# Optimization experiments

Measured on AMD Instinct MI355X. Metric: run time of the kernel, lower is better.

## Reference

```python
import jax, jax.numpy as jnp
import numpy as np

F, E, B = 30, 16, 4096
IN = F * E          # 480 = sum of embed dims
H1, H2 = 1024, 512  # fcn_dims
K = 32              # low-rank adapter k
HH = 512            # hyper hidden dim
D = 3               # domain_num
V = 10000           # vocab per field
EPS = 1e-5


def _bn(h, g, b):
    # BatchNorm1d in training mode: biased batch stats
    mu = h.mean(0)
    var = h.var(0)
    return g * (h - mu) * jax.lax.rsqrt(var + EPS) + b


def setup_inputs() -> dict:
    key = jax.random.key(0)
    ks = jax.random.split(key, 10)
    x = jax.random.randint(ks[0], (F, B), 0, V)
    # last row of x is the domain id, must be in [0, D)
    x = x.at[-1].set(jax.random.randint(ks[1], (B,), 0, D))
    w = lambda k_, s: jax.random.normal(k_, s, jnp.float32) * 0.02
    return {
        "x": x,
        "emb_tables": w(ks[2], (F, V, E)),
        # per-domain MLP (stacked over D): Linear/BN x2 + final Linear(H2->1)
        "dW0": w(ks[3], (D, IN, H1)), "db0": jnp.zeros((D, H1)),
        "dg0": jnp.ones((D, H1)), "dbt0": jnp.zeros((D, H1)),
        "dW1": w(ks[4], (D, H1, H2)), "db1": jnp.zeros((D, H2)),
        "dg1": jnp.ones((D, H2)), "dbt1": jnp.zeros((D, H2)),
        "dWo": w(ks[5], (D, H2, 1)), "dbo": jnp.zeros((D, 1)),
        # hyper_net: Linear+BN+ReLU (IN->HH), Linear+BN+ReLU (HH->K*K)
        "hW0": w(ks[6], (IN, HH)), "hb0": jnp.zeros((HH,)),
        "hg0": jnp.ones((HH,)), "hbt0": jnp.zeros((HH,)),
        "hW1": w(ks[7], (HH, K * K)), "hb1": jnp.zeros((K * K,)),
        "hg1": jnp.ones((K * K,)), "hbt1": jnp.zeros((K * K,)),
        # low-rank factors (torch inits these to ones)
        "u0": jnp.ones((H2, K)), "u1": jnp.ones((32, K)),
        "v0": jnp.ones((K, 32)), "v1": jnp.ones((K, H2)),
        "bl0": jnp.zeros((32,)), "bl1": jnp.zeros((H2,)),
        "gamma1": jnp.ones((H2,)), "bias1": jnp.zeros((H2,)),
    }


def reference(x, emb_tables, dW0, db0, dg0, dbt0, dW1, db1, dg1, dbt1,
              dWo, dbo, hW0, hb0, hg0, hbt0, hW1, hb1, hg1, hbt1,
              u0, u1, v0, v1, bl0, bl1, gamma1, bias1):
    domain_id = x[-1]                                        # [B]
    emb = jax.vmap(lambda t, idx: t[idx])(emb_tables, x)     # [F, B, E]
    emb = emb.transpose(1, 0, 2).reshape(x.shape[1], -1)     # [B, F*E]

    # hyper-net output is identical across the domain loop -> compute once
    h = jax.nn.relu(_bn(emb @ hW0 + hb0, hg0, hbt0))
    h = jax.nn.relu(_bn(h @ hW1 + hb1, hg1, hbt1))
    hyper = h.reshape(-1, K, K)                              # [B, K, K]
    w1 = jnp.einsum('mi,bij,jn->bmn', u0, hyper, v0)         # [B, H2, 32]
    w2 = jnp.einsum('mi,bij,jn->bmn', u1, hyper, v1)         # [B, 32, H2]

    outs = []
    for d in range(D):
        di = jax.nn.relu(_bn(emb @ dW0[d] + db0[d], dg0[d], dbt0[d]))  # [B, H1]
        di = jax.nn.relu(_bn(di @ dW1[d] + db1[d], dg1[d], dbt1[d]))   # [B, H2]
        t = jax.nn.sigmoid(jnp.einsum('bf,bfj->bj', di, w1) + bl0)     # [B, 32]
        t = jnp.einsum('bf,bfj->bj', t, w2) + bl1                      # [B, H2]
        # manual batch-norm with torch.var (unbiased, ddof=1)
        mean, var = t.mean(0), t.var(0, ddof=1)
        out = gamma1 * (t - mean) / jnp.sqrt(var + EPS) + bias1
        di = out + di                                                  # residual
        outs.append(jax.nn.sigmoid(di @ dWo[d] + dbo[d]))              # [B, 1]

    final = jnp.zeros_like(outs[0])
    for d in range(D):
        final = jnp.where((domain_id == d)[:, None], outs[d], final)
    return final
```

## Files before the change

### kernel.cpp

```cpp
#include <hip/hip_runtime.h>
#include <hip/hip_bf16.h>
#include <math.h>

#define F_   30
#define E_   16
#define B_   4096
#define IN_  480
#define H1_  1024
#define H2_  512
#define K_   32
#define HH_  512
#define D_   3
#define V_   10000
#define EPS_ 1e-5f

typedef __attribute__((ext_vector_type(8))) short bf16x8;
typedef __attribute__((ext_vector_type(4))) float f32x4;
typedef __attribute__((ext_vector_type(8))) unsigned short u16x8;

__device__ __forceinline__ unsigned short f2bf(float f) {
    unsigned u = __builtin_bit_cast(unsigned, f);
    u += 0x7FFFu + ((u >> 16) & 1u);
    return (unsigned short)(u >> 16);
}
__device__ __forceinline__ float bf2f(unsigned short h) {
    return __builtin_bit_cast(float, ((unsigned)h) << 16);
}
__device__ __forceinline__ void gload_lds16(const unsigned short* g, unsigned short* l) {
    typedef unsigned int __attribute__((address_space(1))) guint;
    typedef unsigned int __attribute__((address_space(3))) luint;
    __builtin_amdgcn_global_load_lds((const guint*)g, (luint*)l, 16, 0, 0);
}

struct TransArgs {
    const float* src[9];
    unsigned short* dst[9];
    int K[9], N[9], base[9];
};
#define PREP_ZB   73
#define PREP_GA   (PREP_ZB + 960)
#define PREP_TR   (PREP_GA + 3744)
#define PREP_CV   (PREP_TR + 64)
__global__ __launch_bounds__(256) void prep_kernel(TransArgs ta,
                                                   float* __restrict__ zero_p, int zero_n,
                                                   const int* __restrict__ x,
                                                   const float* __restrict__ tables,
                                                   unsigned short* __restrict__ emb,
                                                   const float* __restrict__ v1,
                                                   unsigned short* __restrict__ v1bf) {
    __shared__ float tile[32][33];
    int blk = blockIdx.x;
    int t = threadIdx.x;
    if (blk < PREP_ZB) {
        int i = blk * 256 + t;
        if (i < zero_n) zero_p[i] = 0.f;
    } else if (blk < PREP_GA) {
        int idx = (blk - PREP_ZB) * 256 + t;
        int b = idx / (F_ * 2);
        int r = idx - b * (F_ * 2);
        int f = r >> 1, h = r & 1;
        int row = x[f * B_ + b];
        const float4* src = reinterpret_cast<const float4*>(tables + ((size_t)f * V_ + row) * E_ + h * 8);
        float4 v0 = src[0], v1v = src[1];
        u16x8 o;
        o[0]=f2bf(v0.x); o[1]=f2bf(v0.y); o[2]=f2bf(v0.z); o[3]=f2bf(v0.w);
        o[4]=f2bf(v1v.x); o[5]=f2bf(v1v.y); o[6]=f2bf(v1v.z); o[7]=f2bf(v1v.w);
        *reinterpret_cast<u16x8*>(emb + (size_t)b * IN_ + f * E_ + h * 8) = o;
    } else if (blk < PREP_TR) {
        int gblk = blk - PREP_GA;
        int seg = 0;
#pragma unroll
        for (int i = 1; i < 9; i++) if (gblk >= ta.base[i]) seg = i;
        int tix = gblk - ta.base[seg];
        int Kd = ta.K[seg], Nd = ta.N[seg];
        int tn = Nd >> 5;
        int k0 = (tix / tn) << 5;
        int n0 = (tix - (tix / tn) * tn) << 5;
        const float* src = ta.src[seg];
        unsigned short* dst = ta.dst[seg];
        int c = t & 31, rr = t >> 5;
#pragma unroll
        for (int i = 0; i < 4; i++) {
            int r = rr + i * 8;
            tile[r][c] = src[(size_t)(k0 + r) * Nd + n0 + c];
        }
        __syncthreads();
#pragma unroll
        for (int i = 0; i < 4; i++) {
            int r = rr + i * 8;
            dst[(size_t)(n0 + r) * Kd + k0 + c] = f2bf(tile[c][r]);
        }
    } else {
        int i = (blk - PREP_TR) * 256 + t;
        if (i < K_ * H2_) v1bf[i] = f2bf(v1[i]);
    }
}

struct GemmGroups {
    const unsigned short* A[4];
    const unsigned short* Bt[4];
    void* C[4];
    float* stats[4];
    int N[4], K[4], base[4], obf[4];
};
__global__ __launch_bounds__(256) void gemm_grouped(GemmGroups p) {
    __shared__ unsigned short sA[128 * 32];
    __shared__ unsigned short sB[128 * 32];
    int blk = blockIdx.x;
    int g = 0;
#pragma unroll
    for (int i = 1; i < 4; i++) if (blk >= p.base[i]) g = i;
    int tix = blk - p.base[g];
    int N = p.N[g], K = p.K[g];
    const unsigned short* A = p.A[g];
    const unsigned short* Bt = p.Bt[g];
    float* stats = p.stats[g];
    int bm = (tix & 31) << 7;
    int bn = (tix >> 5) << 7;

    int tid = threadIdx.x;
    int l = tid & 63, w = tid >> 6;
    int wr = w >> 1, wc = w & 1;
    const unsigned short* Ab = A + (size_t)bm * K;
    const unsigned short* Bb = Bt + (size_t)bn * K;
    f32x4 acc[4][4] = {};
    int n0c = tid, n1c = tid + 256;
    int r0 = n0c >> 2, lc0 = (n0c & 3) ^ ((r0 >> 1) & 3);
    int r1 = n1c >> 2, lc1 = (n1c & 3) ^ ((r1 >> 1) & 3);
    int kg = l >> 4, lr = l & 15;
    for (int k0 = 0; k0 < K; k0 += 32) {
        gload_lds16(Ab + (size_t)r0 * K + k0 + lc0 * 8, &sA[n0c * 8]);
        gload_lds16(Ab + (size_t)r1 * K + k0 + lc1 * 8, &sA[n1c * 8]);
        gload_lds16(Bb + (size_t)r0 * K + k0 + lc0 * 8, &sB[n0c * 8]);
        gload_lds16(Bb + (size_t)r1 * K + k0 + lc1 * 8, &sB[n1c * 8]);
        __syncthreads();
        bf16x8 af[4], bfr[4];
#pragma unroll
        for (int m = 0; m < 4; m++) {
            int R = (wr << 6) + (m << 4) + lr;
            af[m] = *reinterpret_cast<const bf16x8*>(&sA[R * 32 + ((kg ^ ((R >> 1) & 3)) << 3)]);
        }
#pragma unroll
        for (int n = 0; n < 4; n++) {
            int R = (wc << 6) + (n << 4) + lr;
            bfr[n] = *reinterpret_cast<const bf16x8*>(&sB[R * 32 + ((kg ^ ((R >> 1) & 3)) << 3)]);
        }
#pragma unroll
        for (int m = 0; m < 4; m++)
#pragma unroll
            for (int n = 0; n < 4; n++)
                acc[m][n] = __builtin_amdgcn_mfma_f32_16x16x32_bf16(af[m], bfr[n], acc[m][n], 0, 0, 0);
        __syncthreads();
    }
    int orow = bm + (wr << 6) + (kg << 2);
    int ocol = bn + (wc << 6) + lr;
    if (p.obf[g]) {
        unsigned short* Cb = (unsigned short*)p.C[g];
#pragma unroll
        for (int m = 0; m < 4; m++)
#pragma unroll
            for (int n = 0; n < 4; n++)
#pragma unroll
                for (int j = 0; j < 4; j++)
                    Cb[(size_t)(orow + (m << 4) + j) * N + ocol + (n << 4)] = f2bf(acc[m][n][j]);
    } else {
        float* C = (float*)p.C[g];
#pragma unroll
        for (int m = 0; m < 4; m++)
#pragma unroll
            for (int n = 0; n < 4; n++)
#pragma unroll
                for (int j = 0; j < 4; j++)
                    C[(size_t)(orow + (m << 4) + j) * N + ocol + (n << 4)] = acc[m][n][j];
    }
#pragma unroll
    for (int n = 0; n < 4; n++) {
        float s = 0.f, ss = 0.f;
#pragma unroll
        for (int m = 0; m < 4; m++)
#pragma unroll
            for (int j = 0; j < 4; j++) {
                float v = acc[m][n][j];
                s += v; ss += v * v;
            }
        s  += __shfl_xor(s, 16);  s  += __shfl_xor(s, 32);
        ss += __shfl_xor(ss, 16); ss += __shfl_xor(ss, 32);
        if (l < 16) {
            int col = bn + (wc << 6) + (n << 4) + lr;
            atomicAdd(&stats[col], s);
            atomicAdd(&stats[N + col], ss);
        }
    }
}

__global__ __launch_bounds__(256) void gemm_bf16_N32(const unsigned short* __restrict__ D1BF,
                                                     const unsigned short* __restrict__ Bt,
                                                     float* __restrict__ Afac) {
    __shared__ unsigned short sA[128 * 32];
    __shared__ unsigned short sB[32 * 32];
    int d = blockIdx.y;
    const unsigned short* A = D1BF + (size_t)d * B_ * H2_;
    float* C = Afac + (size_t)d * B_ * 32;
    const int K = 512;
    int tid = threadIdx.x;
    int l = tid & 63, w = tid >> 6;
    int bm = blockIdx.x << 7;
    const unsigned short* Ab = A + (size_t)bm * K;
    f32x4 acc[2][2] = {};
    int n0c = tid, n1c = tid + 256;
    int r0 = n0c >> 2, lc0 = (n0c & 3) ^ ((r0 >> 1) & 3);
    int r1 = n1c >> 2, lc1 = (n1c & 3) ^ ((r1 >> 1) & 3);
    int kg = l >> 4, lr = l & 15;
    for (int k0 = 0; k0 < K; k0 += 32) {
        gload_lds16(Ab + (size_t)r0 * K + k0 + lc0 * 8, &sA[n0c * 8]);
        gload_lds16(Ab + (size_t)r1 * K + k0 + lc1 * 8, &sA[n1c * 8]);
        if (tid < 128)
            gload_lds16(Bt + (size_t)r0 * K + k0 + lc0 * 8, &sB[n0c * 8]);
        __syncthreads();
        bf16x8 af[2], bfr[2];
#pragma unroll
        for (int m = 0; m < 2; m++) {
            int R = (w << 5) + (m << 4) + lr;
            af[m] = *reinterpret_cast<const bf16x8*>(&sA[R * 32 + ((kg ^ ((R >> 1) & 3)) << 3)]);
        }
#pragma unroll
        for (int n = 0; n < 2; n++) {
            int R = (n << 4) + lr;
            bfr[n] = *reinterpret_cast<const bf16x8*>(&sB[R * 32 + ((kg ^ ((R >> 1) & 3)) << 3)]);
        }
#pragma unroll
        for (int m = 0; m < 2; m++)
#pragma unroll
            for (int n = 0; n < 2; n++)
                acc[m][n] = __builtin_amdgcn_mfma_f32_16x16x32_bf16(af[m], bfr[n], acc[m][n], 0, 0, 0);
        __syncthreads();
    }
    int orow = bm + (w << 5) + (kg << 2);
#pragma unroll
    for (int m = 0; m < 2; m++)
#pragma unroll
        for (int n = 0; n < 2; n++)
#pragma unroll
            for (int j = 0; j < 4; j++)
                C[(size_t)(orow + (m << 4) + j) * 32 + (n << 4) + lr] = acc[m][n][j];
}

__global__ __launch_bounds__(256) void bn480_kernel(const unsigned short* __restrict__ Z480bf,
                                                    const float* __restrict__ stats,
                                                    const float* __restrict__ hg0,
                                                    const float* __restrict__ hbt0,
                                                    const float* __restrict__ dg0,
                                                    const float* __restrict__ dbt0,
                                                    unsigned short* __restrict__ Z0BF,
                                                    unsigned short* __restrict__ ZD0BF) {
    int idx = blockIdx.x * 256 + threadIdx.x;
    int b = idx / 448;
    int c0 = (idx - b * 448) * 8;
    const float* g;
    const float* bt;
    unsigned short* dst;
    if (c0 < 512) {
        g = hg0 + c0; bt = hbt0 + c0;
        dst = Z0BF + (size_t)b * 512 + c0;
    } else {
        int d = (c0 - 512) >> 10, cc = (c0 - 512) & 1023;
        g = dg0 + d * 1024 + cc; bt = dbt0 + d * 1024 + cc;
        dst = ZD0BF + ((size_t)d << 22) + (size_t)b * 1024 + cc;
    }
    u16x8 v = *reinterpret_cast<const u16x8*>(Z480bf + (size_t)b * 3584 + c0);
    u16x8 o;
#pragma unroll
    for (int q = 0; q < 8; q++) {
        float S = stats[c0 + q], SS = stats[3584 + c0 + q];
        float m = S * (1.f / B_);
        float var = (SS - S * m) * (1.f / B_);
        float rs = rsqrtf(var + EPS_);
        o[q] = f2bf(fmaxf(0.f, g[q] * (bf2f(v[q]) - m) * rs + bt[q]));
    }
    *reinterpret_cast<u16x8*>(dst) = o;
}

__global__ __launch_bounds__(256) void bn_l1_kernel(const float* __restrict__ Z1scr,
                                                    const float* __restrict__ SCR1,
                                                    const float* __restrict__ statsH,
                                                    const float* __restrict__ statsD1,
                                                    const float* __restrict__ hg1,
                                                    const float* __restrict__ hbt1,
                                                    const float* __restrict__ dg1,
                                                    const float* __restrict__ dbt1,
                                                    unsigned short* __restrict__ Hbf,
                                                    unsigned short* __restrict__ D1BF) {
    int gidx = blockIdx.x * 256 + threadIdx.x;
    const float* Z; const float* stats; const float* g; const float* bt;
    unsigned short* outp; int c0; int idx;
    if (gidx < 524288) {
        idx = gidx;
        c0 = (idx & 127) * 8;
        Z = Z1scr; stats = statsH; g = hg1; bt = hbt1; outp = Hbf;
    } else {
        idx = gidx - 524288;
        int row = idx >> 6;
        int d = row >> 12;
        c0 = (idx & 63) * 8;
        Z = SCR1; stats = statsD1 + d * 1024; g = dg1 + d * 512; bt = dbt1 + d * 512; outp = D1BF;
    }
    int sh = (gidx < 524288) ? 1024 : 512;
    float4 v0 = reinterpret_cast<const float4*>(Z)[(size_t)idx * 2];
    float4 v1 = reinterpret_cast<const float4*>(Z)[(size_t)idx * 2 + 1];
    float r[8] = {v0.x, v0.y, v0.z, v0.w, v1.x, v1.y, v1.z, v1.w};
    u16x8 o;
#pragma unroll
    for (int q = 0; q < 8; q++) {
        float S = stats[c0 + q], SS = stats[sh + c0 + q];
        float m = S * (1.f / B_);
        float var = (SS - S * m) * (1.f / B_);
        float rs = rsqrtf(var + EPS_);
        o[q] = f2bf(fmaxf(0.f, g[c0 + q] * (r[q] - m) * rs + bt[c0 + q]));
    }
    *reinterpret_cast<u16x8*>(outp + (size_t)idx * 8) = o;
}

__global__ __launch_bounds__(256) void adapter_core(const float* __restrict__ Afac,
                                                    const unsigned short* __restrict__ Hbf,
                                                    const float* __restrict__ v0,
                                                    const float* __restrict__ u1,
                                                    const float* __restrict__ bl0,
                                                    float* __restrict__ C2) {
    __shared__ float sv0[K_ * K_];
    __shared__ float su1[K_ * K_];
    int t = threadIdx.x;
    reinterpret_cast<float4*>(sv0)[t] = reinterpret_cast<const float4*>(v0)[t];
    reinterpret_cast<float4*>(su1)[t] = reinterpret_cast<const float4*>(u1)[t];
    __syncthreads();
    int w = t >> 6, l = t & 63;
    int i = l & 31;
    int b = blockIdx.x * 4 + w;
    float hreg[32];
#pragma unroll
    for (int k = 0; k < 32; k++) hreg[k] = bf2f(Hbf[(size_t)b * 1024 + k * 32 + i]);
    float bl0i = bl0[i];
#pragma unroll
    for (int d = 0; d < 3; d++) {
        float a = Afac[(size_t)d * 131072 + b * 32 + i];
        float c = 0.f;
#pragma unroll
        for (int k = 0; k < 32; k++) c += __shfl(a, k) * hreg[k];
        float targ = bl0i;
#pragma unroll
        for (int k = 0; k < 32; k++) targ += __shfl(c, k) * sv0[k * 32 + i];
        float tv = 1.f / (1.f + expf(-targ));
        float a2 = 0.f;
#pragma unroll
        for (int k = 0; k < 32; k++) a2 += __shfl(tv, k) * su1[k * 32 + i];
        float c2 = 0.f;
#pragma unroll
        for (int k = 0; k < 32; k++) c2 += __shfl(a2, k) * hreg[k];
        if (l < 32) C2[(size_t)d * 131072 + b * 32 + i] = c2;
    }
}

__global__ __launch_bounds__(256) void gram_kernel(const float* __restrict__ C2,
                                                   float* __restrict__ gramM,
                                                   float* __restrict__ gramS) {
    __shared__ float sc[256 * 32];
    int z = blockIdx.y;
    const float* Cz = C2 + (size_t)z * 131072 + (size_t)blockIdx.x * 256 * 32;
    int t = threadIdx.x;
#pragma unroll
    for (int i = 0; i < 8; i++)
        reinterpret_cast<float4*>(sc)[t + i * 256] = reinterpret_cast<const float4*>(Cz)[t + i * 256];
    __syncthreads();
    int k = t >> 3, k4 = (t & 7) << 2;
    float m0 = 0.f, m1 = 0.f, m2 = 0.f, m3 = 0.f;
    for (int r = 0; r < 256; r++) {
        float ck = sc[r * 32 + k];
        m0 += ck * sc[r * 32 + k4 + 0];
        m1 += ck * sc[r * 32 + k4 + 1];
        m2 += ck * sc[r * 32 + k4 + 2];
        m3 += ck * sc[r * 32 + k4 + 3];
    }
    float* Mz = gramM + z * 1024 + k * 32 + k4;
    atomicAdd(&Mz[0], m0); atomicAdd(&Mz[1], m1);
    atomicAdd(&Mz[2], m2); atomicAdd(&Mz[3], m3);
    if (t < 32) {
        float s = 0.f;
        for (int r = 0; r < 256; r++) s += sc[r * 32 + t];
        atomicAdd(&gramS[z * 32 + t], s);
    }
}

__global__ __launch_bounds__(256) void stats_t2_kernel(const float* __restrict__ gramM,
                                                       const float* __restrict__ gramS,
                                                       const unsigned short* __restrict__ v1bf,
                                                       float* __restrict__ statsT2) {
    __shared__ float sM[1024];
    __shared__ float sS[32];
    __shared__ unsigned short sv1[K_ * H2_];
    int z = blockIdx.x;
    int t = threadIdx.x;
    reinterpret_cast<float4*>(sM)[t] = reinterpret_cast<const float4*>(gramM + z * 1024)[t];
    if (t < 8) reinterpret_cast<float4*>(sS)[t] = reinterpret_cast<const float4*>(gramS + z * 32)[t];
#pragma unroll
    for (int i = 0; i < 8; i++)
        reinterpret_cast<u16x8*>(sv1)[t + i * 256] = reinterpret_cast<const u16x8*>(v1bf)[t + i * 256];
    __syncthreads();
#pragma unroll
    for (int jj = 0; jj < 2; jj++) {
        int j = t + jj * 256;
        float vj[32];
#pragma unroll
        for (int k = 0; k < 32; k++) vj[k] = bf2f(sv1[k * 512 + j]);
        float cs = 0.f, ssq = 0.f;
#pragma unroll
        for (int k = 0; k < 32; k++) {
            float wk = 0.f;
#pragma unroll
            for (int kp = 0; kp < 32; kp++) wk += sM[k * 32 + kp] * vj[kp];
            ssq += vj[k] * wk;
            cs += sS[k] * vj[k];
        }
        statsT2[z * 1024 + j] = cs;
        statsT2[z * 1024 + 512 + j] = ssq;
    }
}

__global__ __launch_bounds__(256) void head_kernel(const int* __restrict__ x,
                                                   const float* __restrict__ C2,
                                                   const unsigned short* __restrict__ D1BF,
                                                   const float* __restrict__ statsT2,
                                                   const float* __restrict__ g1,
                                                   const float* __restrict__ b1,
                                                   const float* __restrict__ dWo,
                                                   const float* __restrict__ dbo,
                                                   const unsigned short* __restrict__ v1bf,
                                                   float* __restrict__ out) {
    __shared__ unsigned short sv1[K_ * H2_];
    int t = threadIdx.x;
#pragma unroll
    for (int i = 0; i < 8; i++)
        reinterpret_cast<u16x8*>(sv1)[t + i * 256] = reinterpret_cast<const u16x8*>(v1bf)[t + i * 256];
    __syncthreads();
    int w = t >> 6, l = t & 63;
    int b = blockIdx.x * 4 + w;
    int d = x[(F_ - 1) * B_ + b];
    float cv = C2[((size_t)d * B_ + b) * 32 + (l & 31)];
    float o[8] = {};
#pragma unroll
    for (int k = 0; k < 32; k++) {
        float cb = __shfl(cv, k);
        u16x8 vv = *reinterpret_cast<const u16x8*>(&sv1[k * 512 + l * 8]);
#pragma unroll
        for (int q = 0; q < 8; q++) o[q] += cb * bf2f(vv[q]);
    }
    int j0 = l * 8;
    const float* cs = statsT2 + d * 1024;
    float4 Sa = *reinterpret_cast<const float4*>(cs + j0);
    float4 Sb = *reinterpret_cast<const float4*>(cs + j0 + 4);
    float4 Qa = *reinterpret_cast<const float4*>(cs + 512 + j0);
    float4 Qb = *reinterpret_cast<const float4*>(cs + 512 + j0 + 4);
    float4 Ga = *reinterpret_cast<const float4*>(g1 + j0);
    float4 Gb = *reinterpret_cast<const float4*>(g1 + j0 + 4);
    float4 Ba = *reinterpret_cast<const float4*>(b1 + j0);
    float4 Bb = *reinterpret_cast<const float4*>(b1 + j0 + 4);
    float4 Wa = *reinterpret_cast<const float4*>(dWo + d * 512 + j0);
    float4 Wb = *reinterpret_cast<const float4*>(dWo + d * 512 + j0 + 4);
    u16x8 d1v = *reinterpret_cast<const u16x8*>(D1BF + (size_t)d * 2097152 + (size_t)b * 512 + j0);
    float Sv[8] = {Sa.x,Sa.y,Sa.z,Sa.w,Sb.x,Sb.y,Sb.z,Sb.w};
    float Qv[8] = {Qa.x,Qa.y,Qa.z,Qa.w,Qb.x,Qb.y,Qb.z,Qb.w};
    float Gv[8] = {Ga.x,Ga.y,Ga.z,Ga.w,Gb.x,Gb.y,Gb.z,Gb.w};
    float Bv[8] = {Ba.x,Ba.y,Ba.z,Ba.w,Bb.x,Bb.y,Bb.z,Bb.w};
    float Wv[8] = {Wa.x,Wa.y,Wa.z,Wa.w,Wb.x,Wb.y,Wb.z,Wb.w};
    float p = 0.f;
#pragma unroll
    for (int q = 0; q < 8; q++) {
        float S = Sv[q], SS = Qv[q];
        float m = S * (1.f / B_);
        float var = (SS - S * m) * (1.f / (B_ - 1));
        float rs = rsqrtf(var + EPS_);
        float di = Gv[q] * (o[q] - m) * rs + Bv[q] + bf2f(d1v[q]);
        p += di * Wv[q];
    }
    p += __shfl_down(p, 32); p += __shfl_down(p, 16); p += __shfl_down(p, 8);
    p += __shfl_down(p, 4);  p += __shfl_down(p, 2);  p += __shfl_down(p, 1);
    if (l == 0) out[b] = 1.f / (1.f + expf(-(p + dbo[d])));
}

extern "C" void kernel_launch(void* const* d_in, const int* in_sizes, int n_in,
                              void* d_out, int out_size, void* d_ws, size_t ws_size,
                              hipStream_t stream) {
    const int*   x      = (const int*)  d_in[0];
    const float* tables = (const float*)d_in[1];
    const float* dW0  = (const float*)d_in[2];
    const float* dg0  = (const float*)d_in[4];
    const float* dbt0 = (const float*)d_in[5];
    const float* dW1  = (const float*)d_in[6];
    const float* dg1  = (const float*)d_in[8];
    const float* dbt1 = (const float*)d_in[9];
    const float* dWo  = (const float*)d_in[10];
    const float* dbo  = (const float*)d_in[11];
    const float* hW0  = (const float*)d_in[12];
    const float* hg0  = (const float*)d_in[14];
    const float* hbt0 = (const float*)d_in[15];
    const float* hW1  = (const float*)d_in[16];
    const float* hg1  = (const float*)d_in[18];
    const float* hbt1 = (const float*)d_in[19];
    const float* u0   = (const float*)d_in[20];
    const float* u1   = (const float*)d_in[21];
    const float* v0   = (const float*)d_in[22];
    const float* v1   = (const float*)d_in[23];
    const float* bl0  = (const float*)d_in[24];
    const float* g1   = (const float*)d_in[26];
    const float* b1   = (const float*)d_in[27];
    float* out = (float*)d_out;

    float* ws       = (float*)d_ws;
    float* stats480 = ws;
    float* statsH   = stats480 + 7168;
    float* statsD1  = statsH + 2048;
    float* statsT2  = statsD1 + 3072;
    float* gramM    = statsT2 + 3072;
    float* gramS    = gramM + 3072;
    float* Afac     = ws + 18560;
    float* C2       = Afac + 393216;
    float* Z1scr    = C2 + 393216;
    float* SCR1     = Z1scr + 4194304;
    unsigned short* Z480bf = (unsigned short*)(SCR1 + 6291456);
    unsigned short* embBF = Z480bf + 14680064;
    unsigned short* Z0BF  = embBF + 1966080;
    unsigned short* ZD0BF = Z0BF + 2097152;
    unsigned short* Hbf   = ZD0BF + 12582912;
    unsigned short* D1BF  = Hbf + 4194304;
    unsigned short* W480  = D1BF + 6291456;
    unsigned short* hW1t  = W480 + 1720320;
    unsigned short* dW1t  = hW1t + 524288;
    unsigned short* u0t   = dW1t + 1572864;
    unsigned short* v1bf  = u0t + 16384;

    TransArgs ta;
    ta.src[0] = hW0; ta.dst[0] = W480; ta.K[0] = 480; ta.N[0] = 512;
    ta.src[1] = hW1; ta.dst[1] = hW1t; ta.K[1] = 512; ta.N[1] = 1024;
    for (int d = 0; d < 3; d++) {
        ta.src[2 + d] = dW0 + (size_t)d * 480 * 1024;
        ta.dst[2 + d] = W480 + (size_t)(512 + d * 1024) * 480;
        ta.K[2 + d] = 480; ta.N[2 + d] = 1024;
        ta.src[5 + d] = dW1 + (size_t)d * 1024 * 512;
        ta.dst[5 + d] = dW1t + (size_t)d * 512 * 1024;
        ta.K[5 + d] = 1024; ta.N[5 + d] = 512;
    }
    ta.src[8] = u0; ta.dst[8] = u0t; ta.K[8] = 512; ta.N[8] = 32;
    int acc_t = 0;
    for (int i = 0; i < 9; i++) { ta.base[i] = acc_t; acc_t += (ta.K[i] >> 5) * (ta.N[i] >> 5); }

    prep_kernel<<<PREP_CV, 256, 0, stream>>>(ta, ws, 18560, x, tables, embBF, v1, v1bf);

    GemmGroups g480;
    g480.A[0] = embBF; g480.Bt[0] = W480; g480.C[0] = Z480bf;
    g480.stats[0] = stats480; g480.N[0] = 3584; g480.K[0] = 480; g480.base[0] = 0; g480.obf[0] = 1;
    for (int i = 1; i < 4; i++) { g480.base[i] = 0x7fffffff; g480.A[i] = nullptr; g480.Bt[i] = nullptr; g480.C[i] = nullptr; g480.stats[i] = nullptr; g480.N[i] = 0; g480.K[i] = 32; g480.obf[i] = 0; }
    gemm_grouped<<<896, 256, 0, stream>>>(g480);
    bn480_kernel<<<7168, 256, 0, stream>>>(Z480bf, stats480, hg0, hbt0, dg0, dbt0, Z0BF, ZD0BF);

    GemmGroups g2;
    g2.A[0] = Z0BF; g2.Bt[0] = hW1t; g2.C[0] = Z1scr;
    g2.stats[0] = statsH; g2.N[0] = 1024; g2.K[0] = 512; g2.base[0] = 0; g2.obf[0] = 0;
    for (int d = 0; d < 3; d++) {
        g2.A[1 + d] = ZD0BF + (size_t)d * 4194304;
        g2.Bt[1 + d] = dW1t + (size_t)d * 524288;
        g2.C[1 + d] = SCR1 + (size_t)d * 2097152;
        g2.stats[1 + d] = statsD1 + d * 1024;
        g2.N[1 + d] = 512; g2.K[1 + d] = 1024;
        g2.base[1 + d] = 256 + d * 128;
        g2.obf[1 + d] = 0;
    }
    gemm_grouped<<<640, 256, 0, stream>>>(g2);
    bn_l1_kernel<<<5120, 256, 0, stream>>>(Z1scr, SCR1, statsH, statsD1, hg1, hbt1, dg1, dbt1, Hbf, D1BF);

    gemm_bf16_N32<<<dim3(32, 3), 256, 0, stream>>>(D1BF, u0t, Afac);
    adapter_core<<<1024, 256, 0, stream>>>(Afac, Hbf, v0, u1, bl0, C2);
    gram_kernel<<<dim3(16, 3), 256, 0, stream>>>(C2, gramM, gramS);
    stats_t2_kernel<<<3, 256, 0, stream>>>(gramM, gramS, v1bf, statsT2);
    head_kernel<<<1024, 256, 0, stream>>>(x, C2, D1BF, statsT2, g1, b1, dWo, dbo, v1bf, out);
    (void)in_sizes; (void)n_in; (void)out_size; (void)ws_size;
}
```

Baseline: 283.9 us.

## Fuse first-layer batchnorm+ReLU into second-layer GEMM A-operand load

Removes the standalone bn480 kernel and applies the layer-0 BatchNorm affine and ReLU while loading the A tile inside a new grouped GEMM, which reads the raw 3584-wide Z480 buffer directly. The second GEMM now writes bf16 outputs instead of fp32 scratch, and bn_l1 reads bf16, halving that intermediate traffic. The cost is that A loads become plain register loads plus on-the-fly math instead of async LDS copies, and BN applied after the bf16 store adds rounding.

After: 272.1 us. 4.1% less time.

```diff
diff --git a/kernel.cpp b/kernel.cpp
--- a/kernel.cpp
+++ b/kernel.cpp
@@ -193,6 +193,117 @@
     }
 }
 
+struct L1Groups {
+    const unsigned short* Bt[4];
+    unsigned short* C[4];
+    float* stats[4];
+    const float* gg[4];
+    const float* gb[4];
+    int N[4], K[4], base[4], colbase[4];
+};
+__global__ __launch_bounds__(256) void gemm_l1(L1Groups p,
+                                               const unsigned short* __restrict__ Z480bf,
+                                               const float* __restrict__ stats480) {
+    __shared__ unsigned short sA[128 * 32];
+    __shared__ unsigned short sB[128 * 32];
+    __shared__ float2 aff[1024];
+    int blk = blockIdx.x;
+    int g = 0;
+#pragma unroll
+    for (int i = 1; i < 4; i++) if (blk >= p.base[i]) g = i;
+    int tix = blk - p.base[g];
+    int N = p.N[g], K = p.K[g], colbase = p.colbase[g];
+    const unsigned short* Bt = p.Bt[g];
+    float* stats = p.stats[g];
+    const float* gg = p.gg[g];
+    const float* gb = p.gb[g];
+    int tid = threadIdx.x;
+    for (int k = tid; k < K; k += 256) {
+        int col = colbase + k;
+        float S = stats480[col], SS = stats480[3584 + col];
+        float m = S * (1.f / B_);
+        float var = (SS - S * m) * (1.f / B_);
+        float rs = rsqrtf(var + EPS_);
+        float s = gg[k] * rs;
+        aff[k] = make_float2(s, gb[k] - m * s);
+    }
+    int bm = (tix & 31) << 7;
+    int bn = (tix >> 5) << 7;
+    const unsigned short* Bb = Bt + (size_t)bn * K;
+    int l = tid & 63, w = tid >> 6;
+    int wr = w >> 1, wc = w & 1;
+    f32x4 acc[4][4] = {};
+    int n0c = tid, n1c = tid + 256;
+    int r0 = n0c >> 2, lc0 = (n0c & 3) ^ ((r0 >> 1) & 3);
+    int r1 = n1c >> 2, lc1 = (n1c & 3) ^ ((r1 >> 1) & 3);
+    int kg = l >> 4, lr = l & 15;
+    const unsigned short* Arow0 = Z480bf + (size_t)(bm + r0) * 3584 + colbase + lc0 * 8;
+    const unsigned short* Arow1 = Z480bf + (size_t)(bm + r1) * 3584 + colbase + lc1 * 8;
+    __syncthreads();
+    for (int k0 = 0; k0 < K; k0 += 32) {
+        gload_lds16(Bb + (size_t)r0 * K + k0 + lc0 * 8, &sB[n0c * 8]);
+        gload_lds16(Bb + (size_t)r1 * K + k0 + lc1 * 8, &sB[n1c * 8]);
+        u16x8 za = *reinterpret_cast<const u16x8*>(Arow0 + k0);
+        u16x8 zb = *reinterpret_cast<const u16x8*>(Arow1 + k0);
+        u16x8 oa, ob;
+#pragma unroll
+        for (int q = 0; q < 8; q++) {
+            float2 pa = aff[k0 + lc0 * 8 + q];
+            oa[q] = f2bf(fmaxf(0.f, bf2f(za[q]) * pa.x + pa.y));
+            float2 pb = aff[k0 + lc1 * 8 + q];
+            ob[q] = f2bf(fmaxf(0.f, bf2f(zb[q]) * pb.x + pb.y));
+        }
+        *reinterpret_cast<u16x8*>(&sA[n0c * 8]) = oa;
+        *reinterpret_cast<u16x8*>(&sA[n1c * 8]) = ob;
+        __syncthreads();
+        bf16x8 af[4], bfr[4];
+#pragma unroll
+        for (int m = 0; m < 4; m++) {
+            int R = (wr << 6) + (m << 4) + lr;
+            af[m] = *reinterpret_cast<const bf16x8*>(&sA[R * 32 + ((kg ^ ((R >> 1) & 3)) << 3)]);
+        }
+#pragma unroll
+        for (int n = 0; n < 4; n++) {
+            int R = (wc << 6) + (n << 4) + lr;
+            bfr[n] = *reinterpret_cast<const bf16x8*>(&sB[R * 32 + ((kg ^ ((R >> 1) & 3)) << 3)]);
+        }
+#pragma unroll
+        for (int m = 0; m < 4; m++)
+#pragma unroll
+            for (int n = 0; n < 4; n++)
+                acc[m][n] = __builtin_amdgcn_mfma_f32_16x16x32_bf16(af[m], bfr[n], acc[m][n], 0, 0, 0);
+        __syncthreads();
+    }
+    int orow = bm + (wr << 6) + (kg << 2);
+    int ocol = bn + (wc << 6) + lr;
+    unsigned short* Cb = p.C[g];
+#pragma unroll
+    for (int m = 0; m < 4; m++)
+#pragma unroll
+        for (int n = 0; n < 4; n++)
+#pragma unroll
+            for (int j = 0; j < 4; j++)
+                Cb[(size_t)(orow + (m << 4) + j) * N + ocol + (n << 4)] = f2bf(acc[m][n][j]);
+#pragma unroll
+    for (int n = 0; n < 4; n++) {
+        float s = 0.f, ss = 0.f;
+#pragma unroll
+        for (int m = 0; m < 4; m++)
+#pragma unroll
+            for (int j = 0; j < 4; j++) {
+                float v = acc[m][n][j];
+                s += v; ss += v * v;
+            }
+        s  += __shfl_xor(s, 16);  s  += __shfl_xor(s, 32);
+        ss += __shfl_xor(ss, 16); ss += __shfl_xor(ss, 32);
+        if (l < 16) {
+            int col = bn + (wc << 6) + (n << 4) + lr;
+            atomicAdd(&stats[col], s);
+            atomicAdd(&stats[N + col], ss);
+        }
+    }
+}
+
 __global__ __launch_bounds__(256) void gemm_bf16_N32(const unsigned short* __restrict__ D1BF,
                                                      const unsigned short* __restrict__ Bt,
                                                      float* __restrict__ Afac) {
@@ -245,43 +356,8 @@
                 C[(size_t)(orow + (m << 4) + j) * 32 + (n << 4) + lr] = acc[m][n][j];
 }
 
-__global__ __launch_bounds__(256) void bn480_kernel(const unsigned short* __restrict__ Z480bf,
-                                                    const float* __restrict__ stats,
-                                                    const float* __restrict__ hg0,
-                                                    const float* __restrict__ hbt0,
-                                                    const float* __restrict__ dg0,
-                                                    const float* __restrict__ dbt0,
-                                                    unsigned short* __restrict__ Z0BF,
-                                                    unsigned short* __restrict__ ZD0BF) {
-    int idx = blockIdx.x * 256 + threadIdx.x;
-    int b = idx / 448;
-    int c0 = (idx - b * 448) * 8;
-    const float* g;
-    const float* bt;
-    unsigned short* dst;
-    if (c0 < 512) {
-        g = hg0 + c0; bt = hbt0 + c0;
-        dst = Z0BF + (size_t)b * 512 + c0;
-    } else {
-        int d = (c0 - 512) >> 10, cc = (c0 - 512) & 1023;
-        g = dg0 + d * 1024 + cc; bt = dbt0 + d * 1024 + cc;
-        dst = ZD0BF + ((size_t)d << 22) + (size_t)b * 1024 + cc;
-    }
-    u16x8 v = *reinterpret_cast<const u16x8*>(Z480bf + (size_t)b * 3584 + c0);
-    u16x8 o;
-#pragma unroll
-    for (int q = 0; q < 8; q++) {
-        float S = stats[c0 + q], SS = stats[3584 + c0 + q];
-        float m = S * (1.f / B_);
-        float var = (SS - S * m) * (1.f / B_);
-        float rs = rsqrtf(var + EPS_);
-        o[q] = f2bf(fmaxf(0.f, g[q] * (bf2f(v[q]) - m) * rs + bt[q]));
-    }
-    *reinterpret_cast<u16x8*>(dst) = o;
-}
-
-__global__ __launch_bounds__(256) void bn_l1_kernel(const float* __restrict__ Z1scr,
-                                                    const float* __restrict__ SCR1,
+__global__ __launch_bounds__(256) void bn_l1_kernel(const unsigned short* __restrict__ Z1BF,
+                                                    const unsigned short* __restrict__ SD1BF,
                                                     const float* __restrict__ statsH,
                                                     const float* __restrict__ statsD1,
                                                     const float* __restrict__ hg1,
@@ -291,23 +367,21 @@
                                                     unsigned short* __restrict__ Hbf,
                                                     unsigned short* __restrict__ D1BF) {
     int gidx = blockIdx.x * 256 + threadIdx.x;
-    const float* Z; const float* stats; const float* g; const float* bt;
+    const unsigned short* Z; const float* stats; const float* g; const float* bt;
     unsigned short* outp; int c0; int idx;
     if (gidx < 524288) {
         idx = gidx;
         c0 = (idx & 127) * 8;
-        Z = Z1scr; stats = statsH; g = hg1; bt = hbt1; outp = Hbf;
+        Z = Z1BF; stats = statsH; g = hg1; bt = hbt1; outp = Hbf;
     } else {
         idx = gidx - 524288;
         int row = idx >> 6;
         int d = row >> 12;
         c0 = (idx & 63) * 8;
-        Z = SCR1; stats = statsD1 + d * 1024; g = dg1 + d * 512; bt = dbt1 + d * 512; outp = D1BF;
+        Z = SD1BF; stats = statsD1 + d * 1024; g = dg1 + d * 512; bt = dbt1 + d * 512; outp = D1BF;
     }
     int sh = (gidx < 524288) ? 1024 : 512;
-    float4 v0 = reinterpret_cast<const float4*>(Z)[(size_t)idx * 2];
-    float4 v1 = reinterpret_cast<const float4*>(Z)[(size_t)idx * 2 + 1];
-    float r[8] = {v0.x, v0.y, v0.z, v0.w, v1.x, v1.y, v1.z, v1.w};
+    u16x8 v = *reinterpret_cast<const u16x8*>(Z + (size_t)idx * 8);
     u16x8 o;
 #pragma unroll
     for (int q = 0; q < 8; q++) {
@@ -315,7 +389,7 @@
         float m = S * (1.f / B_);
         float var = (SS - S * m) * (1.f / B_);
         float rs = rsqrtf(var + EPS_);
-        o[q] = f2bf(fmaxf(0.f, g[c0 + q] * (r[q] - m) * rs + bt[c0 + q]));
+        o[q] = f2bf(fmaxf(0.f, g[c0 + q] * (bf2f(v[q]) - m) * rs + bt[c0 + q]));
     }
     *reinterpret_cast<u16x8*>(outp + (size_t)idx * 8) = o;
 }
@@ -522,13 +596,11 @@
     float* gramS    = gramM + 3072;
     float* Afac     = ws + 18560;
     float* C2       = Afac + 393216;
-    float* Z1scr    = C2 + 393216;
-    float* SCR1     = Z1scr + 4194304;
-    unsigned short* Z480bf = (unsigned short*)(SCR1 + 6291456);
+    unsigned short* Z480bf = (unsigned short*)(C2 + 393216);
     unsigned short* embBF = Z480bf + 14680064;
-    unsigned short* Z0BF  = embBF + 1966080;
-    unsigned short* ZD0BF = Z0BF + 2097152;
-    unsigned short* Hbf   = ZD0BF + 12582912;
+    unsigned short* Z1BF  = embBF + 1966080;
+    unsigned short* SD1BF = Z1BF + 4194304;
+    unsigned short* Hbf   = SD1BF + 6291456;
     unsigned short* D1BF  = Hbf + 4194304;
     unsigned short* W480  = D1BF + 6291456;
     unsigned short* hW1t  = W480 + 1720320;
@@ -558,22 +630,23 @@
     g480.stats[0] = stats480; g480.N[0] = 3584; g480.K[0] = 480; g480.base[0] = 0; g480.obf[0] = 1;
     for (int i = 1; i < 4; i++) { g480.base[i] = 0x7fffffff; g480.A[i] = nullptr; g480.Bt[i] = nullptr; g480.C[i] = nullptr; g480.stats[i] = nullptr; g480.N[i] = 0; g480.K[i] = 32; g480.obf[i] = 0; }
     gemm_grouped<<<896, 256, 0, stream>>>(g480);
-    bn480_kernel<<<7168, 256, 0, stream>>>(Z480bf, stats480, hg0, hbt0, dg0, dbt0, Z0BF, ZD0BF);
-
-    GemmGroups g2;
-    g2.A[0] = Z0BF; g2.Bt[0] = hW1t; g2.C[0] = Z1scr;
-    g2.stats[0] = statsH; g2.N[0] = 1024; g2.K[0] = 512; g2.base[0] = 0; g2.obf[0] = 0;
+
+    L1Groups gl;
     for (int d = 0; d < 3; d++) {
-        g2.A[1 + d] = ZD0BF + (size_t)d * 4194304;
-        g2.Bt[1 + d] = dW1t + (size_t)d * 524288;
-        g2.C[1 + d] = SCR1 + (size_t)d * 2097152;
-        g2.stats[1 + d] = statsD1 + d * 1024;
-        g2.N[1 + d] = 512; g2.K[1 + d] = 1024;
-        g2.base[1 + d] = 256 + d * 128;
-        g2.obf[1 + d] = 0;
-    }
-    gemm_grouped<<<640, 256, 0, stream>>>(g2);
-    bn_l1_kernel<<<5120, 256, 0, stream>>>(Z1scr, SCR1, statsH, statsD1, hg1, hbt1, dg1, dbt1, Hbf, D1BF);
+        gl.Bt[d] = dW1t + (size_t)d * 524288;
+        gl.C[d] = SD1BF + (size_t)d * 2097152;
+        gl.stats[d] = statsD1 + d * 1024;
+        gl.gg[d] = dg0 + d * 1024; gl.gb[d] = dbt0 + d * 1024;
+        gl.N[d] = 512; gl.K[d] = 1024;
+        gl.base[d] = d * 128;
+        gl.colbase[d] = 512 + d * 1024;
+    }
+    gl.Bt[3] = hW1t; gl.C[3] = Z1BF; gl.stats[3] = statsH;
+    gl.gg[3] = hg0; gl.gb[3] = hbt0;
+    gl.N[3] = 1024; gl.K[3] = 512; gl.base[3] = 384; gl.colbase[3] = 0;
+    gemm_l1<<<640, 256, 0, stream>>>(gl, Z480bf, stats480);
+
+    bn_l1_kernel<<<5120, 256, 0, stream>>>(Z1BF, SD1BF, statsH, statsD1, hg1, hbt1, dg1, dbt1, Hbf, D1BF);
 
     gemm_bf16_N32<<<dim3(32, 3), 256, 0, stream>>>(D1BF, u0t, Afac);
     adapter_core<<<1024, 256, 0, stream>>>(Afac, Hbf, v0, u1, bl0, C2);
```
